# Optimization experiments

Hardware: AMD Instinct MI355X
Metric: run time of the kernel (lower is better)

## Reference

```python
import jax, jax.numpy as jnp
import numpy as np

N_MELS, HIDDEN, HEAD_DIM = 80, 128, 64


def _gru_step(h, gx_t, w_hh, b_hh):
    # PyTorch GRU cell math. gx_t = x_t @ W_ih^T + b_ih, precomputed. [B, 3H]
    H = h.shape[-1]
    gh = h @ w_hh.T + b_hh  # [B, 3H]
    r = jax.nn.sigmoid(gx_t[:, :H] + gh[:, :H])
    z = jax.nn.sigmoid(gx_t[:, H:2 * H] + gh[:, H:2 * H])
    n = jnp.tanh(gx_t[:, 2 * H:] + r * gh[:, 2 * H:])
    return (1.0 - z) * n + z * h


def setup_inputs() -> dict:
    key = jax.random.key(0)
    ks = jax.random.split(key, 14)
    s = 1.0 / np.sqrt(HIDDEN)
    u = lambda k, shape, sc: jax.random.uniform(k, shape, jnp.float32, -sc, sc)
    return {
        "x": jax.random.normal(ks[0], (128, 1500, N_MELS), dtype=jnp.float32),
        # forward-direction GRU params
        "w_ih_f": u(ks[1], (3 * HIDDEN, N_MELS), s),
        "w_hh_f": u(ks[2], (3 * HIDDEN, HIDDEN), s),
        "b_ih_f": u(ks[3], (3 * HIDDEN,), s),
        "b_hh_f": u(ks[4], (3 * HIDDEN,), s),
        # backward-direction GRU params
        "w_ih_b": u(ks[5], (3 * HIDDEN, N_MELS), s),
        "w_hh_b": u(ks[6], (3 * HIDDEN, HIDDEN), s),
        "b_ih_b": u(ks[7], (3 * HIDDEN,), s),
        "b_hh_b": u(ks[8], (3 * HIDDEN,), s),
        # MLP head: Linear(2H, 64) -> ReLU -> Linear(64, 1)
        "w1": u(ks[9], (HEAD_DIM, 2 * HIDDEN), 1.0 / np.sqrt(2 * HIDDEN)),
        "b1": u(ks[10], (HEAD_DIM,), 1.0 / np.sqrt(2 * HIDDEN)),
        "w2": u(ks[11], (1, HEAD_DIM), 1.0 / np.sqrt(HEAD_DIM)),
        "b2": u(ks[12], (1,), 1.0 / np.sqrt(HEAD_DIM)),
    }


def reference(x, w_ih_f, w_hh_f, b_ih_f, b_hh_f, w_ih_b, w_hh_b, b_ih_b, b_hh_b, w1, b1, w2, b2):
    B, T, _ = x.shape
    h0 = jnp.zeros((B, HIDDEN), dtype=x.dtype)

    # Forward direction: last output = final hidden state after full scan.
    # Precompute input projections for all timesteps in one GEMM.
    gx_f = jnp.einsum('bti,gi->tbg', x, w_ih_f) + b_ih_f  # [T, B, 3H]
    h_f, _ = jax.lax.scan(lambda h, g: (_gru_step(h, g, w_hh_f, b_hh_f), None), h0, gx_f)

    # Backward direction: out[:, -1, H:] in PyTorch is the backward hidden
    # after processing ONLY x[:, -1] (the reverse scan's first step), so a
    # single GRU step from h0 reproduces it exactly.
    gx_b_last = x[:, -1, :] @ w_ih_b.T + b_ih_b  # [B, 3H]
    h_b = _gru_step(h0, gx_b_last, w_hh_b, b_hh_b)

    last = jnp.concatenate([h_f, h_b], axis=-1)  # [B, 2H]
    # Head (eval mode: dropout is identity)
    hdn = jax.nn.relu(last @ w1.T + b1)
    out = hdn @ w2.T + b2  # [B, 1]
    return out[:, 0]
```

## Files before the change

kernel.cpp:

```cpp
#include <hip/hip_runtime.h>

#define B 128
#define T 1500
#define NI 80
#define H 128
#define G 384
#define TT 64

typedef float v2f __attribute__((ext_vector_type(2)));

__device__ __forceinline__ float sigf(float x) { return 1.0f / (1.0f + __expf(-x)); }
__device__ __forceinline__ float tanhfast(float x) { return 1.0f - 2.0f / (1.0f + __expf(2.0f * x)); }
__device__ __forceinline__ v2f pkfma(v2f a, v2f b, v2f c) { return __builtin_elementwise_fma(a, b, c); }

__global__ __launch_bounds__(384)
void gx_gemm_kernel(const float* __restrict__ x, const float* __restrict__ w_ih,
                    const float* __restrict__ b_ih, float* __restrict__ gx,
                    int t0, int ct) {
    int tile = blockIdx.x;
    int b = blockIdx.y;
    int tl0 = tile * TT;
    if (tl0 >= ct) return;
    int n = (ct - tl0 < TT) ? (ct - tl0) : TT;
    int tid = threadIdx.x;

    __shared__ __align__(16) float xs[TT * NI];
    const float4* xsrc4 = (const float4*)(x + ((size_t)b * T + (size_t)(t0 + tl0)) * NI);
    int total4 = n * (NI / 4);
    for (int i = tid; i < total4; i += 384) ((float4*)xs)[i] = xsrc4[i];

    v2f w2[40];
    const v2f* wr = (const v2f*)(w_ih + (size_t)tid * NI);
#pragma unroll
    for (int i = 0; i < 40; ++i) w2[i] = wr[i];
    float bias = b_ih[tid];
    __syncthreads();

    float* gout = gx + ((size_t)b * ct + (size_t)tl0) * G + tid;
    int tt = 0;
    for (; tt + 2 <= n; tt += 2) {
        const float4* xa4 = (const float4*)(xs + tt * NI);
        const float4* xb4 = (const float4*)(xs + (tt + 1) * NI);
        v2f a0 = {0.f, 0.f}, a1 = {0.f, 0.f}, c0 = {0.f, 0.f}, c1 = {0.f, 0.f};
#pragma unroll
        for (int i = 0; i < 20; ++i) {
            float4 xa = xa4[i];
            float4 xb = xb4[i];
            v2f alo = {xa.x, xa.y}, ahi = {xa.z, xa.w};
            v2f blo = {xb.x, xb.y}, bhi = {xb.z, xb.w};
            a0 = pkfma(w2[2 * i], alo, a0);
            a1 = pkfma(w2[2 * i + 1], ahi, a1);
            c0 = pkfma(w2[2 * i], blo, c0);
            c1 = pkfma(w2[2 * i + 1], bhi, c1);
        }
        gout[(size_t)tt * G]       = bias + ((a0.x + a0.y) + (a1.x + a1.y));
        gout[(size_t)(tt + 1) * G] = bias + ((c0.x + c0.y) + (c1.x + c1.y));
    }
    if (tt < n) {
        const float4* xa4 = (const float4*)(xs + tt * NI);
        v2f a0 = {0.f, 0.f}, a1 = {0.f, 0.f};
#pragma unroll
        for (int i = 0; i < 20; ++i) {
            float4 xa = xa4[i];
            v2f alo = {xa.x, xa.y}, ahi = {xa.z, xa.w};
            a0 = pkfma(w2[2 * i], alo, a0);
            a1 = pkfma(w2[2 * i + 1], ahi, a1);
        }
        gout[(size_t)tt * G] = bias + ((a0.x + a0.y) + (a1.x + a1.y));
    }
}

__global__ __launch_bounds__(512)
void scan_kernel(const float* __restrict__ gx, const float* __restrict__ w_hh,
                 const float* __restrict__ b_hh, float* __restrict__ h_state,
                 int ct, int first, int last,
                 const float* __restrict__ x,
                 const float* __restrict__ w_ih_b, const float* __restrict__ b_ih_b,
                 const float* __restrict__ b_hh_b,
                 const float* __restrict__ w1, const float* __restrict__ b1,
                 const float* __restrict__ w2, const float* __restrict__ b2,
                 float* __restrict__ out) {
    int b = blockIdx.x;
    int tid = threadIdx.x;
    int j = tid >> 2;
    int q = tid & 3;
    int jpad = j + ((j >> 5) << 2);

    __shared__ __align__(16) float hs0[144];
    __shared__ __align__(16) float hs1[144];
    __shared__ __align__(16) float tail_gx[G];
    __shared__ __align__(16) float last_s[2 * H];
    __shared__ __align__(16) float xb_s[NI];

    v2f WR[16], WZ[16], WN[16];
    {
        const v2f* p0 = (const v2f*)(w_hh + (size_t)j * H + 32 * q);
        const v2f* p1 = (const v2f*)(w_hh + (size_t)(j + H) * H + 32 * q);
        const v2f* p2 = (const v2f*)(w_hh + (size_t)(j + 2 * H) * H + 32 * q);
#pragma unroll
        for (int i = 0; i < 16; ++i) { WR[i] = p0[i]; WZ[i] = p1[i]; WN[i] = p2[i]; }
    }
    float br = b_hh[j], bz = b_hh[j + H], bn = b_hh[j + 2 * H];

    float h_cur = 0.f;
    if (!first) h_cur = h_state[b * H + j];
    if (q == 0) hs0[jpad] = h_cur;

    float ga0, ga1, ga2, gb0 = 0.f, gb1 = 0.f, gb2 = 0.f;
    {
        const float* gp = gx + (size_t)b * ct * G;
        ga0 = gp[j]; ga1 = gp[j + H]; ga2 = gp[j + 2 * H];
        if (ct > 1) { gb0 = gp[G + j]; gb1 = gp[G + j + H]; gb2 = gp[G + j + 2 * H]; }
    }
    asm volatile("s_waitcnt lgkmcnt(0)\n\ts_barrier" ::: "memory");

    auto step = [&](int TL, const float* SRC, float* DST, float& g0, float& g1, float& g2) {
        const float4* hv4 = (const float4*)(SRC + 36 * q);
        v2f arv = {0.f, 0.f}, azv = {0.f, 0.f}, anv = {0.f, 0.f};
#pragma unroll
        for (int i = 0; i < 8; ++i) {
            float4 hv = hv4[i];
            v2f hlo = {hv.x, hv.y}, hhi = {hv.z, hv.w};
            arv = pkfma(WR[2 * i], hlo, arv);
            azv = pkfma(WZ[2 * i], hlo, azv);
            anv = pkfma(WN[2 * i], hlo, anv);
            arv = pkfma(WR[2 * i + 1], hhi, arv);
            azv = pkfma(WZ[2 * i + 1], hhi, azv);
            anv = pkfma(WN[2 * i + 1], hhi, anv);
        }
        float ar = arv.x + arv.y, az = azv.x + azv.y, an = anv.x + anv.y;
        ar += __shfl_xor(ar, 1); az += __shfl_xor(az, 1); an += __shfl_xor(an, 1);
        ar += __shfl_xor(ar, 2); az += __shfl_xor(az, 2); an += __shfl_xor(an, 2);
        float r = sigf(g0 + br + ar);
        float z = sigf(g1 + bz + az);
        float n = tanhfast(g2 + r * (bn + an));
        h_cur = (1.f - z) * n + z * h_cur;
        if (q == 0) DST[jpad] = h_cur;
        if (TL + 2 < ct) {
            const float* gp = gx + ((size_t)b * ct + TL + 2) * G;
            g0 = gp[j]; g1 = gp[j + H]; g2 = gp[j + 2 * H];
        }
        asm volatile("s_waitcnt lgkmcnt(0)\n\ts_barrier" ::: "memory");
    };

    int tl = 0;
    for (; tl + 1 < ct; tl += 2) {
        step(tl,     hs0, hs1, ga0, ga1, ga2);
        step(tl + 1, hs1, hs0, gb0, gb1, gb2);
    }
    if (tl < ct) step(tl, hs0, hs1, ga0, ga1, ga2);

    if (!last) {
        if (q == 0) h_state[b * H + j] = h_cur;
        return;
    }

    if (tid < NI) xb_s[tid] = x[((size_t)b * T + (T - 1)) * NI + tid];
    if (q == 0) last_s[j] = h_cur;
    __syncthreads();

    if (tid < G) {
        const float4* wbr = (const float4*)(w_ih_b + (size_t)tid * NI);
        const float4* xv = (const float4*)xb_s;
        float a0 = 0.f, a1 = 0.f, a2 = 0.f, a3 = 0.f;
#pragma unroll
        for (int i = 0; i < 20; ++i) {
            float4 wv = wbr[i]; float4 x4 = xv[i];
            a0 = fmaf(wv.x, x4.x, a0); a1 = fmaf(wv.y, x4.y, a1);
            a2 = fmaf(wv.z, x4.z, a2); a3 = fmaf(wv.w, x4.w, a3);
        }
        tail_gx[tid] = b_ih_b[tid] + ((a0 + a1) + (a2 + a3));
    }
    __syncthreads();

    if (tid < H) {
        float r = sigf(tail_gx[tid] + b_hh_b[tid]);
        float z = sigf(tail_gx[tid + H] + b_hh_b[tid + H]);
        float n = tanhfast(tail_gx[tid + 2 * H] + r * b_hh_b[tid + 2 * H]);
        last_s[H + tid] = (1.f - z) * n;
    }
    __syncthreads();

    if (tid < 64) {
        const float4* w1r = (const float4*)(w1 + (size_t)tid * 2 * H);
        const float4* lv = (const float4*)last_s;
        float a0 = 0.f, a1 = 0.f, a2 = 0.f, a3 = 0.f;
#pragma unroll
        for (int i = 0; i < 64; ++i) {
            float4 wv = w1r[i]; float4 l4 = lv[i];
            a0 = fmaf(wv.x, l4.x, a0); a1 = fmaf(wv.y, l4.y, a1);
            a2 = fmaf(wv.z, l4.z, a2); a3 = fmaf(wv.w, l4.w, a3);
        }
        float v = b1[tid] + ((a0 + a1) + (a2 + a3));
        v = fmaxf(v, 0.f) * w2[tid];
#pragma unroll
        for (int off = 32; off > 0; off >>= 1) v += __shfl_down(v, off);
        if (tid == 0) out[b] = v + b2[0];
    }
}

extern "C" void kernel_launch(void* const* d_in, const int* in_sizes, int n_in,
                              void* d_out, int out_size, void* d_ws, size_t ws_size,
                              hipStream_t stream) {
    (void)in_sizes; (void)n_in; (void)out_size;
    const float* x      = (const float*)d_in[0];
    const float* w_ih_f = (const float*)d_in[1];
    const float* w_hh_f = (const float*)d_in[2];
    const float* b_ih_f = (const float*)d_in[3];
    const float* b_hh_f = (const float*)d_in[4];
    const float* w_ih_b = (const float*)d_in[5];
    const float* w_hh_b = (const float*)d_in[6];
    const float* b_ih_b = (const float*)d_in[7];
    const float* b_hh_b = (const float*)d_in[8];
    const float* w1     = (const float*)d_in[9];
    const float* b1     = (const float*)d_in[10];
    const float* w2     = (const float*)d_in[11];
    const float* b2     = (const float*)d_in[12];
    (void)w_hh_b;
    float* out = (float*)d_out;

    float* h_state = (float*)d_ws;
    float* gxbuf = h_state + B * H;
    size_t hbytes = (size_t)B * H * sizeof(float);
    size_t avail = ws_size > hbytes ? ws_size - hbytes : 0;
    long long chunkT = (long long)(avail / ((size_t)B * G * sizeof(float)));
    if (chunkT > T) chunkT = T;
    if (chunkT < 1) chunkT = 1;

    for (int t0 = 0; t0 < T; t0 += (int)chunkT) {
        int ct = (T - t0 < (int)chunkT) ? (T - t0) : (int)chunkT;
        int ntiles = (ct + TT - 1) / TT;
        gx_gemm_kernel<<<dim3(ntiles, B), dim3(384), 0, stream>>>(
            x, w_ih_f, b_ih_f, gxbuf, t0, ct);
        scan_kernel<<<dim3(B), dim3(512), 0, stream>>>(
            gxbuf, w_hh_f, b_hh_f, h_state, ct,
            (t0 == 0) ? 1 : 0, (t0 + ct >= T) ? 1 : 0,
            x, w_ih_b, b_ih_b, b_hh_b, w1, b1, w2, b2, out);
    }
}
```

Measured before the change: 1.163 ms.

## Split recurrent GEMV across 8 lanes per hidden pair with DPP reductions

Rebuilds the GRU scan's thread mapping so each group of 8 lanes computes two hidden units, each lane covering 16 columns of h for six weight rows. This reduces LDS reads of h per step and replaces the shuffle-based cross-lane reduction with DPP row operations. The padded shared h layout changes to 20-float strides to avoid bank conflicts. Each lane now does redundant reductions for both units, and the DPP control masks have to be correct for the 8-lane groups.

```diff
diff --git a/kernel.cpp b/kernel.cpp
--- a/kernel.cpp
+++ b/kernel.cpp
@@ -12,6 +12,18 @@
 __device__ __forceinline__ float sigf(float x) { return 1.0f / (1.0f + __expf(-x)); }
 __device__ __forceinline__ float tanhfast(float x) { return 1.0f - 2.0f / (1.0f + __expf(2.0f * x)); }
 __device__ __forceinline__ v2f pkfma(v2f a, v2f b, v2f c) { return __builtin_elementwise_fma(a, b, c); }
+
+__device__ __forceinline__ float sum8(float v) {
+    int a = __builtin_bit_cast(int, v);
+    float m = __builtin_bit_cast(float, __builtin_amdgcn_update_dpp(0, a, 0x141, 0xF, 0xF, true));
+    float s = v + m;
+    a = __builtin_bit_cast(int, s);
+    m = __builtin_bit_cast(float, __builtin_amdgcn_update_dpp(0, a, 0x1B, 0xF, 0xF, true));
+    s = s + m;
+    a = __builtin_bit_cast(int, s);
+    m = __builtin_bit_cast(float, __builtin_amdgcn_update_dpp(0, a, 0xB1, 0xF, 0xF, true));
+    return s + m;
+}
 
 __global__ __launch_bounds__(384)
 void gx_gemm_kernel(const float* __restrict__ x, const float* __restrict__ w_ih,
@@ -82,81 +94,114 @@
                  float* __restrict__ out) {
     int b = blockIdx.x;
     int tid = threadIdx.x;
-    int j = tid >> 2;
-    int q = tid & 3;
-    int jpad = j + ((j >> 5) << 2);
-
-    __shared__ __align__(16) float hs0[144];
-    __shared__ __align__(16) float hs1[144];
+    int jp = tid >> 3;
+    int q = tid & 7;
+    int j0 = jp, j1 = jp + 64;
+    int jsel = (q < 4) ? j0 : j1;
+    int hsel = ((jsel >> 4) * 20) + (jsel & 15);
+    bool writer = (q & 3) == 0;
+
+    __shared__ __align__(16) float hs[2][160];
     __shared__ __align__(16) float tail_gx[G];
     __shared__ __align__(16) float last_s[2 * H];
     __shared__ __align__(16) float xb_s[NI];
 
-    v2f WR[16], WZ[16], WN[16];
+    float4 W0r[4], W0z[4], W0n[4], W1r[4], W1z[4], W1n[4];
     {
-        const v2f* p0 = (const v2f*)(w_hh + (size_t)j * H + 32 * q);
-        const v2f* p1 = (const v2f*)(w_hh + (size_t)(j + H) * H + 32 * q);
-        const v2f* p2 = (const v2f*)(w_hh + (size_t)(j + 2 * H) * H + 32 * q);
-#pragma unroll
-        for (int i = 0; i < 16; ++i) { WR[i] = p0[i]; WZ[i] = p1[i]; WN[i] = p2[i]; }
-    }
-    float br = b_hh[j], bz = b_hh[j + H], bn = b_hh[j + 2 * H];
+        const float* wb = w_hh + 16 * q;
+        const float4* p0 = (const float4*)(wb + (size_t)j0 * H);
+        const float4* p1 = (const float4*)(wb + (size_t)(j0 + H) * H);
+        const float4* p2 = (const float4*)(wb + (size_t)(j0 + 2 * H) * H);
+        const float4* p3 = (const float4*)(wb + (size_t)j1 * H);
+        const float4* p4 = (const float4*)(wb + (size_t)(j1 + H) * H);
+        const float4* p5 = (const float4*)(wb + (size_t)(j1 + 2 * H) * H);
+#pragma unroll
+        for (int i = 0; i < 4; ++i) {
+            W0r[i] = p0[i]; W0z[i] = p1[i]; W0n[i] = p2[i];
+            W1r[i] = p3[i]; W1z[i] = p4[i]; W1n[i] = p5[i];
+        }
+    }
+    float br = b_hh[jsel], bz = b_hh[jsel + H], bn = b_hh[jsel + 2 * H];
 
     float h_cur = 0.f;
-    if (!first) h_cur = h_state[b * H + j];
-    if (q == 0) hs0[jpad] = h_cur;
+    if (!first) h_cur = h_state[b * H + jsel];
+    if (writer) hs[0][hsel] = h_cur;
 
     float ga0, ga1, ga2, gb0 = 0.f, gb1 = 0.f, gb2 = 0.f;
     {
         const float* gp = gx + (size_t)b * ct * G;
-        ga0 = gp[j]; ga1 = gp[j + H]; ga2 = gp[j + 2 * H];
-        if (ct > 1) { gb0 = gp[G + j]; gb1 = gp[G + j + H]; gb2 = gp[G + j + 2 * H]; }
-    }
-    asm volatile("s_waitcnt lgkmcnt(0)\n\ts_barrier" ::: "memory");
-
-    auto step = [&](int TL, const float* SRC, float* DST, float& g0, float& g1, float& g2) {
-        const float4* hv4 = (const float4*)(SRC + 36 * q);
-        v2f arv = {0.f, 0.f}, azv = {0.f, 0.f}, anv = {0.f, 0.f};
-#pragma unroll
-        for (int i = 0; i < 8; ++i) {
-            float4 hv = hv4[i];
-            v2f hlo = {hv.x, hv.y}, hhi = {hv.z, hv.w};
-            arv = pkfma(WR[2 * i], hlo, arv);
-            azv = pkfma(WZ[2 * i], hlo, azv);
-            anv = pkfma(WN[2 * i], hlo, anv);
-            arv = pkfma(WR[2 * i + 1], hhi, arv);
-            azv = pkfma(WZ[2 * i + 1], hhi, azv);
-            anv = pkfma(WN[2 * i + 1], hhi, anv);
-        }
-        float ar = arv.x + arv.y, az = azv.x + azv.y, an = anv.x + anv.y;
-        ar += __shfl_xor(ar, 1); az += __shfl_xor(az, 1); an += __shfl_xor(an, 1);
-        ar += __shfl_xor(ar, 2); az += __shfl_xor(az, 2); an += __shfl_xor(an, 2);
+        ga0 = gp[jsel]; ga1 = gp[jsel + H]; ga2 = gp[jsel + 2 * H];
+        if (ct > 1) { gb0 = gp[G + jsel]; gb1 = gp[G + jsel + H]; gb2 = gp[G + jsel + 2 * H]; }
+    }
+    __syncthreads();
+
+    auto step = [&](int TL, int SB, float& g0, float& g1, float& g2) {
+        const float4* hv4 = (const float4*)(&hs[SB][0] + 20 * q);
+        float4 h0 = hv4[0], h1 = hv4[1], h2 = hv4[2], h3 = hv4[3];
+        v2f a0r = {0.f, 0.f}, a0z = {0.f, 0.f}, a0n = {0.f, 0.f};
+        v2f a1r = {0.f, 0.f}, a1z = {0.f, 0.f}, a1n = {0.f, 0.f};
+        v2f hl, hh;
+        hl = v2f{h0.x, h0.y}; hh = v2f{h0.z, h0.w};
+        a0r = pkfma(v2f{W0r[0].x, W0r[0].y}, hl, a0r); a0r = pkfma(v2f{W0r[0].z, W0r[0].w}, hh, a0r);
+        a0z = pkfma(v2f{W0z[0].x, W0z[0].y}, hl, a0z); a0z = pkfma(v2f{W0z[0].z, W0z[0].w}, hh, a0z);
+        a0n = pkfma(v2f{W0n[0].x, W0n[0].y}, hl, a0n); a0n = pkfma(v2f{W0n[0].z, W0n[0].w}, hh, a0n);
+        a1r = pkfma(v2f{W1r[0].x, W1r[0].y}, hl, a1r); a1r = pkfma(v2f{W1r[0].z, W1r[0].w}, hh, a1r);
+        a1z = pkfma(v2f{W1z[0].x, W1z[0].y}, hl, a1z); a1z = pkfma(v2f{W1z[0].z, W1z[0].w}, hh, a1z);
+        a1n = pkfma(v2f{W1n[0].x, W1n[0].y}, hl, a1n); a1n = pkfma(v2f{W1n[0].z, W1n[0].w}, hh, a1n);
+        hl = v2f{h1.x, h1.y}; hh = v2f{h1.z, h1.w};
+        a0r = pkfma(v2f{W0r[1].x, W0r[1].y}, hl, a0r); a0r = pkfma(v2f{W0r[1].z, W0r[1].w}, hh, a0r);
+        a0z = pkfma(v2f{W0z[1].x, W0z[1].y}, hl, a0z); a0z = pkfma(v2f{W0z[1].z, W0z[1].w}, hh, a0z);
+        a0n = pkfma(v2f{W0n[1].x, W0n[1].y}, hl, a0n); a0n = pkfma(v2f{W0n[1].z, W0n[1].w}, hh, a0n);
+        a1r = pkfma(v2f{W1r[1].x, W1r[1].y}, hl, a1r); a1r = pkfma(v2f{W1r[1].z, W1r[1].w}, hh, a1r);
+        a1z = pkfma(v2f{W1z[1].x, W1z[1].y}, hl, a1z); a1z = pkfma(v2f{W1z[1].z, W1z[1].w}, hh, a1z);
+        a1n = pkfma(v2f{W1n[1].x, W1n[1].y}, hl, a1n); a1n = pkfma(v2f{W1n[1].z, W1n[1].w}, hh, a1n);
+        hl = v2f{h2.x, h2.y}; hh = v2f{h2.z, h2.w};
+        a0r = pkfma(v2f{W0r[2].x, W0r[2].y}, hl, a0r); a0r = pkfma(v2f{W0r[2].z, W0r[2].w}, hh, a0r);
+        a0z = pkfma(v2f{W0z[2].x, W0z[2].y}, hl, a0z); a0z = pkfma(v2f{W0z[2].z, W0z[2].w}, hh, a0z);
+        a0n = pkfma(v2f{W0n[2].x, W0n[2].y}, hl, a0n); a0n = pkfma(v2f{W0n[2].z, W0n[2].w}, hh, a0n);
+        a1r = pkfma(v2f{W1r[2].x, W1r[2].y}, hl, a1r); a1r = pkfma(v2f{W1r[2].z, W1r[2].w}, hh, a1r);
+        a1z = pkfma(v2f{W1z[2].x, W1z[2].y}, hl, a1z); a1z = pkfma(v2f{W1z[2].z, W1z[2].w}, hh, a1z);
+        a1n = pkfma(v2f{W1n[2].x, W1n[2].y}, hl, a1n); a1n = pkfma(v2f{W1n[2].z, W1n[2].w}, hh, a1n);
+        hl = v2f{h3.x, h3.y}; hh = v2f{h3.z, h3.w};
+        a0r = pkfma(v2f{W0r[3].x, W0r[3].y}, hl, a0r); a0r = pkfma(v2f{W0r[3].z, W0r[3].w}, hh, a0r);
+        a0z = pkfma(v2f{W0z[3].x, W0z[3].y}, hl, a0z); a0z = pkfma(v2f{W0z[3].z, W0z[3].w}, hh, a0z);
+        a0n = pkfma(v2f{W0n[3].x, W0n[3].y}, hl, a0n); a0n = pkfma(v2f{W0n[3].z, W0n[3].w}, hh, a0n);
+        a1r = pkfma(v2f{W1r[3].x, W1r[3].y}, hl, a1r); a1r = pkfma(v2f{W1r[3].z, W1r[3].w}, hh, a1r);
+        a1z = pkfma(v2f{W1z[3].x, W1z[3].y}, hl, a1z); a1z = pkfma(v2f{W1z[3].z, W1z[3].w}, hh, a1z);
+        a1n = pkfma(v2f{W1n[3].x, W1n[3].y}, hl, a1n); a1n = pkfma(v2f{W1n[3].z, W1n[3].w}, hh, a1n);
+
+        float s0r = sum8(a0r.x + a0r.y), s0z = sum8(a0z.x + a0z.y), s0n = sum8(a0n.x + a0n.y);
+        float s1r = sum8(a1r.x + a1r.y), s1z = sum8(a1z.x + a1z.y), s1n = sum8(a1n.x + a1n.y);
+        bool lo = q < 4;
+        float ar = lo ? s0r : s1r;
+        float az = lo ? s0z : s1z;
+        float an = lo ? s0n : s1n;
         float r = sigf(g0 + br + ar);
         float z = sigf(g1 + bz + az);
         float n = tanhfast(g2 + r * (bn + an));
-        h_cur = (1.f - z) * n + z * h_cur;
-        if (q == 0) DST[jpad] = h_cur;
+        h_cur = n + z * (h_cur - n);
+        if (writer) hs[SB ^ 1][hsel] = h_cur;
         if (TL + 2 < ct) {
             const float* gp = gx + ((size_t)b * ct + TL + 2) * G;
-            g0 = gp[j]; g1 = gp[j + H]; g2 = gp[j + 2 * H];
+            g0 = gp[jsel]; g1 = gp[jsel + H]; g2 = gp[jsel + 2 * H];
         }
         asm volatile("s_waitcnt lgkmcnt(0)\n\ts_barrier" ::: "memory");
     };
 
     int tl = 0;
     for (; tl + 1 < ct; tl += 2) {
-        step(tl,     hs0, hs1, ga0, ga1, ga2);
-        step(tl + 1, hs1, hs0, gb0, gb1, gb2);
-    }
-    if (tl < ct) step(tl, hs0, hs1, ga0, ga1, ga2);
+        step(tl,     0, ga0, ga1, ga2);
+        step(tl + 1, 1, gb0, gb1, gb2);
+    }
+    if (tl < ct) step(tl, 0, ga0, ga1, ga2);
 
     if (!last) {
-        if (q == 0) h_state[b * H + j] = h_cur;
+        if (writer) h_state[b * H + jsel] = h_cur;
         return;
     }
 
     if (tid < NI) xb_s[tid] = x[((size_t)b * T + (T - 1)) * NI + tid];
-    if (q == 0) last_s[j] = h_cur;
+    if (writer) last_s[jsel] = h_cur;
     __syncthreads();
 
     if (tid < G) {
```

Measured after the change: 1.151 ms. No clear change (-1.1%).
